# Optimization experiments

Measured on AMD Instinct MI355X. Metric: run time of the kernel, lower is better.

The kernel has to match this reference:

```python
import jax, jax.numpy as jnp
import numpy as np

NA = 100000
NB = 100000
N_REL = 6
REL_SRC = ['A', 'B', 'A', 'B', 'A', 'B']
REL_DST = ['B', 'A', 'A', 'B', 'B', 'A']
N_NODES = {'A': NA, 'B': NB}
H_DIM, OUT_DIM, N_BASES, N_EDGES = 64, 16, 4, 500000


def setup_inputs() -> dict:
    key = jax.random.key(0)
    ks = jax.random.split(key, 16)
    inp = {
        'embed_A': jax.random.normal(ks[0], (NA, H_DIM), jnp.float32) * 0.1,
        'embed_B': jax.random.normal(ks[1], (NB, H_DIM), jnp.float32) * 0.1,
        'bias0': jnp.zeros((H_DIM,), jnp.float32),
        'w_comp1': jax.random.normal(ks[2], (N_REL, N_BASES), jnp.float32) * 0.5,
        'basis1': jax.random.normal(ks[3], (N_BASES, H_DIM, H_DIM), jnp.float32) * (1.0 / np.sqrt(H_DIM)),
        'bias1': jnp.zeros((H_DIM,), jnp.float32),
        'w_comp2': jax.random.normal(ks[4], (N_REL, N_BASES), jnp.float32) * 0.5,
        'basis2': jax.random.normal(ks[5], (N_BASES, H_DIM, OUT_DIM), jnp.float32) * (1.0 / np.sqrt(H_DIM)),
        'bias2': jnp.zeros((OUT_DIM,), jnp.float32),
    }
    for r in range(N_REL):
        inp[f'src_r{r}'] = jax.random.randint(ks[6 + r], (N_EDGES,), 0, N_NODES[REL_SRC[r]], jnp.int32)
        inp[f'dst_r{r}'] = jax.random.randint(jax.random.fold_in(ks[6 + r], 7), (N_EDGES,), 0, N_NODES[REL_DST[r]], jnp.int32)
    return inp


def _hetero_conv(h, W_rels, bias, edges, out_dim, activation):
    # h: dict ntype -> [N, d_in]; W_rels: None or [n_rel, d_in, d_out]
    out = {nt: jnp.zeros((N_NODES[nt], out_dim), h['A'].dtype) for nt in N_NODES}
    for r in range(N_REL):
        src_t, dst_t = REL_SRC[r], REL_DST[r]
        src, dst = edges[r]
        x = h[src_t] if W_rels is None else h[src_t] @ W_rels[r]  # [N_src, d_out]
        msg = x[src]  # gather: [E, d_out]
        n_dst = N_NODES[dst_t]
        agg = jax.ops.segment_sum(msg, dst, num_segments=n_dst)
        deg = jax.ops.segment_sum(jnp.ones((msg.shape[0],), msg.dtype), dst, num_segments=n_dst)
        out[dst_t] = out[dst_t] + agg / jnp.maximum(deg, 1.0)[:, None]  # norm='right'
    out = {nt: out[nt] + bias for nt in out}
    if activation is not None:
        out = {nt: activation(out[nt]) for nt in out}
    return out


def reference(embed_A, embed_B, bias0, w_comp1, basis1, bias1, w_comp2, basis2, bias2,
              src_r0, dst_r0, src_r1, dst_r1, src_r2, dst_r2,
              src_r3, dst_r3, src_r4, dst_r4, src_r5, dst_r5):
    edges = [(src_r0, dst_r0), (src_r1, dst_r1), (src_r2, dst_r2),
             (src_r3, dst_r3), (src_r4, dst_r4), (src_r5, dst_r5)]
    h = {'A': embed_A, 'B': embed_B}
    # layer 0: weight=False -> pure normalized aggregation + bias + relu
    h = _hetero_conv(h, None, bias0, edges, H_DIM, jax.nn.relu)
    # hidden layer with basis-decomposed weights
    W1 = jnp.einsum('rb,bio->rio', w_comp1, basis1)
    h = _hetero_conv(h, W1, bias1, edges, H_DIM, jax.nn.relu)
    # output layer, no activation
    W2 = jnp.einsum('rb,bio->rio', w_comp2, basis2)
    h = _hetero_conv(h, W2, bias2, edges, OUT_DIM, None)
    return h['A']  # logits for category node type
```

## Files before the change

kernel.cpp:

```cpp
#include <hip/hip_runtime.h>

#define NN 100000
#define EE 500000
#define DD 64
#define OD 16
#define NR 6
#define NBASE 4
#define BSH 10
#define NBK 98
#define SBLK 128
#define FLATN (NBK * SBLK)
#define STCAP 5632
#define DBIN 64
#define DBLK 128
#define FLAT2 (DBIN * DBLK)
#define NVR 8

struct Edges { const int* src[NR]; const int* dst[NR]; };

typedef __attribute__((ext_vector_type(8))) short bf16x8;
typedef __attribute__((ext_vector_type(4))) float f32x4;

__device__ __forceinline__ float bf2f(ushort u) {
    union { unsigned int i; float f; } v; v.i = ((unsigned int)u) << 16; return v.f;
}
__device__ __forceinline__ ushort f2bf(float f) {
    unsigned int x = __float_as_uint(f);
    unsigned int r = (x + 0x7fffu + ((x >> 16) & 1u)) >> 16;
    return (ushort)r;
}
__device__ __forceinline__ void bfpair(unsigned int u, float& lo, float& hi) {
    lo = __uint_as_float(u << 16);
    hi = __uint_as_float(u & 0xffff0000u);
}

__global__ __launch_bounds__(256) void build_w_kernel(
    const float* __restrict__ wc1, const float* __restrict__ b1,
    const float* __restrict__ wc2, const float* __restrict__ b2,
    ushort* __restrict__ Wp1, ushort* __restrict__ Wp2)
{
    int idx = blockIdx.x * blockDim.x + threadIdx.x;
    const int n1 = NR * DD * DD;
    const int n2 = NR * DD * OD;
    if (idx < n1) {
        int r = idx >> 12, rem = idx & 4095;
        int i = rem >> 6, o = rem & 63;
        float s = 0.f;
        #pragma unroll
        for (int b = 0; b < NBASE; ++b) s += wc1[r * NBASE + b] * b1[b * 4096 + rem];
        Wp1[(((size_t)(r * 8 + (i >> 3)) * 64 + o) << 3) + (i & 7)] = f2bf(s);
    } else if (idx < n1 + n2) {
        int j = idx - n1;
        int r = j >> 10, rem = j & 1023;
        int i = rem >> 4, o = rem & 15;
        float s = 0.f;
        #pragma unroll
        for (int b = 0; b < NBASE; ++b) s += wc2[r * NBASE + b] * b2[b * 1024 + rem];
        Wp2[(((size_t)(r * 8 + (i >> 3)) * 16 + o) << 3) + (i & 7)] = f2bf(s);
    }
}

__global__ __launch_bounds__(256) void cvt_kernel(
    const float* __restrict__ in, ushort* __restrict__ out, int n4)
{
    int i = blockIdx.x * 256 + threadIdx.x;
    if (i >= n4) return;
    float4 v = ((const float4*)in)[i];
    ushort4 o;
    o.x = f2bf(v.x); o.y = f2bf(v.y); o.z = f2bf(v.z); o.w = f2bf(v.w);
    ((ushort4*)out)[i] = o;
}

__global__ __launch_bounds__(256) void count_kernel(Edges ep, int* __restrict__ cnt_mat)
{
    __shared__ int h[NBK];
    int r = blockIdx.y, blk = blockIdx.x;
    const int* __restrict__ dst = ep.dst[r];
    const int chunk = (EE + SBLK - 1) / SBLK;
    int e0 = blk * chunk, e1 = min(e0 + chunk, EE);
    for (int i = threadIdx.x; i < NBK; i += 256) h[i] = 0;
    __syncthreads();
    for (int e = e0 + threadIdx.x; e < e1; e += 256)
        atomicAdd(&h[dst[e] >> BSH], 1);
    __syncthreads();
    for (int b = threadIdx.x; b < NBK; b += 256)
        cnt_mat[r * FLATN + b * SBLK + blk] = h[b];
}

__global__ __launch_bounds__(1024) void flat_scan_kernel(
    const int* __restrict__ cnt_mat, int* __restrict__ off_flat, int* __restrict__ bbase)
{
    __shared__ int wsum[16];
    const int TPE = 13;
    int r = blockIdx.x;
    int tid = threadIdx.x, lane = tid & 63, wid = tid >> 6;
    int base = tid * TPE;
    int v[TPE];
    int s = 0;
    #pragma unroll
    for (int j = 0; j < TPE; ++j) {
        int i = base + j;
        v[j] = (i < FLATN) ? cnt_mat[r * FLATN + i] : 0;
        s += v[j];
    }
    int si = s;
    #pragma unroll
    for (int off = 1; off < 64; off <<= 1) {
        int t = __shfl_up(si, off);
        if (lane >= off) si += t;
    }
    if (lane == 63) wsum[wid] = si;
    __syncthreads();
    if (wid == 0) {
        int ws = (lane < 16) ? wsum[lane] : 0;
        #pragma unroll
        for (int off = 1; off < 16; off <<= 1) {
            int t = __shfl_up(ws, off);
            if (lane >= off) ws += t;
        }
        if (lane < 16) wsum[lane] = ws;
    }
    __syncthreads();
    int texcl = (wid > 0 ? wsum[wid - 1] : 0) + (si - s);
    int part = 0;
    #pragma unroll
    for (int j = 0; j < TPE; ++j) {
        int i = base + j;
        if (i < FLATN) {
            int o = texcl + part;
            off_flat[r * FLATN + i] = o;
            if ((i & (SBLK - 1)) == 0) bbase[r * (NBK + 1) + (i >> 7)] = o;
        }
        part += v[j];
    }
    if (tid == 0) bbase[r * (NBK + 1) + NBK] = EE;
}

__global__ __launch_bounds__(256) void scatter2_kernel(
    Edges ep, const int* __restrict__ off_flat, unsigned int* __restrict__ ebuf)
{
    __shared__ int goff[NBK];
    __shared__ int lcnt[NBK];
    int r = blockIdx.y, blk = blockIdx.x;
    const int* __restrict__ src = ep.src[r];
    const int* __restrict__ dst = ep.dst[r];
    unsigned int* eb = ebuf + (size_t)r * EE;
    const int chunk = (EE + SBLK - 1) / SBLK;
    int e0 = blk * chunk, e1 = min(e0 + chunk, EE);
    if (threadIdx.x < NBK) {
        goff[threadIdx.x] = off_flat[r * FLATN + threadIdx.x * SBLK + blk];
        lcnt[threadIdx.x] = 0;
    }
    __syncthreads();
    for (int e = e0 + threadIdx.x; e < e1; e += 256) {
        int d = dst[e];
        int b = d >> BSH;
        int pos = goff[b] + atomicAdd(&lcnt[b], 1);
        eb[pos] = (unsigned int)src[e] | ((unsigned int)(d & 1023) << 17);
    }
}

__global__ __launch_bounds__(256) void csr_fine_kernel(
    const unsigned int* __restrict__ ebuf, const int* __restrict__ bbase,
    int* __restrict__ row_ptr, float* __restrict__ inv_deg, int* __restrict__ col_idx)
{
    __shared__ int nh[1024];
    __shared__ int nb[1024];
    __shared__ int wsum4[4];
    __shared__ int stage[STCAP];
    int r = blockIdx.y, b = blockIdx.x;
    int tid = threadIdx.x, lane = tid & 63, wid = tid >> 6;
    int gb = bbase[r * (NBK + 1) + b];
    int ge = bbase[r * (NBK + 1) + b + 1];
    int cnt = ge - gb;
    if (cnt > STCAP) cnt = STCAP;
    const unsigned int* eb = ebuf + (size_t)r * EE + gb;
    #pragma unroll
    for (int j = 0; j < 4; ++j) nh[tid * 4 + j] = 0;
    __syncthreads();
    for (int i = tid; i < cnt; i += 256)
        atomicAdd(&nh[(eb[i] >> 17) & 1023], 1);
    __syncthreads();
    int v0 = nh[tid * 4 + 0], v1 = nh[tid * 4 + 1], v2 = nh[tid * 4 + 2], v3 = nh[tid * 4 + 3];
    int s = v0 + v1 + v2 + v3;
    int si = s;
    #pragma unroll
    for (int off = 1; off < 64; off <<= 1) {
        int t = __shfl_up(si, off);
        if (lane >= off) si += t;
    }
    if (lane == 63) wsum4[wid] = si;
    __syncthreads();
    if (tid == 0) {
        int a = 0;
        #pragma unroll
        for (int k = 0; k < 4; ++k) { int t = wsum4[k]; wsum4[k] = a; a += t; }
    }
    __syncthreads();
    int texcl = wsum4[wid] + (si - s);
    int p0 = texcl, p1 = p0 + v0, p2 = p1 + v1, p3 = p2 + v2;
    nb[tid * 4 + 0] = p0; nb[tid * 4 + 1] = p1; nb[tid * 4 + 2] = p2; nb[tid * 4 + 3] = p3;
    {
        int node0 = b * 1024 + tid * 4;
        int pj[4] = { p0, p1, p2, p3 };
        int vj[4] = { v0, v1, v2, v3 };
        #pragma unroll
        for (int j = 0; j < 4; ++j) {
            int node = node0 + j;
            if (node < NN) {
                row_ptr[r * (NN + 1) + node] = gb + pj[j];
                inv_deg[r * NN + node] = 1.0f / (float)(vj[j] > 1 ? vj[j] : 1);
            }
        }
    }
    if (b == NBK - 1 && tid == 0) row_ptr[r * (NN + 1) + NN] = EE;
    #pragma unroll
    for (int j = 0; j < 4; ++j) nh[tid * 4 + j] = 0;
    __syncthreads();
    for (int i = tid; i < cnt; i += 256) {
        unsigned int w = eb[i];
        int loc = (w >> 17) & 1023;
        int pos = nb[loc] + atomicAdd(&nh[loc], 1);
        stage[pos] = (int)(w & 0x1ffffu);
    }
    __syncthreads();
    int* co = col_idx + (size_t)r * EE + gb;
    for (int i = tid; i < cnt; i += 256) co[i] = stage[i];
}

__device__ __forceinline__ int vdeg(int vr, int n, const int* __restrict__ rp)
{
    if (vr < 6) return rp[vr * (NN + 1) + n + 1] - rp[vr * (NN + 1) + n];
    if (vr == 6)
        return (rp[1 * (NN + 1) + n + 1] - rp[1 * (NN + 1) + n])
             + (rp[2 * (NN + 1) + n + 1] - rp[2 * (NN + 1) + n])
             + (rp[5 * (NN + 1) + n + 1] - rp[5 * (NN + 1) + n]);
    return (rp[0 * (NN + 1) + n + 1] - rp[0 * (NN + 1) + n])
         + (rp[3 * (NN + 1) + n + 1] - rp[3 * (NN + 1) + n])
         + (rp[4 * (NN + 1) + n + 1] - rp[4 * (NN + 1) + n]);
}

__global__ __launch_bounds__(256) void dhist_kernel(
    const int* __restrict__ row_ptr, int* __restrict__ cnt2)
{
    __shared__ int h[DBIN];
    int vr = blockIdx.y, blk = blockIdx.x;
    if (threadIdx.x < DBIN) h[threadIdx.x] = 0;
    __syncthreads();
    const int chunk = (NN + DBLK - 1) / DBLK;
    int n0 = blk * chunk, n1 = min(n0 + chunk, NN);
    for (int n = n0 + threadIdx.x; n < n1; n += 256)
        atomicAdd(&h[min(vdeg(vr, n, row_ptr), DBIN - 1)], 1);
    __syncthreads();
    if (threadIdx.x < DBIN) cnt2[vr * FLAT2 + threadIdx.x * DBLK + blk] = h[threadIdx.x];
}

__global__ __launch_bounds__(1024) void dscan_kernel(
    const int* __restrict__ cnt2, int* __restrict__ off2)
{
    __shared__ int wsum[16];
    const int TPE = 8;
    int vr = blockIdx.x;
    int tid = threadIdx.x, lane = tid & 63, wid = tid >> 6;
    int base = tid * TPE;
    int v[TPE];
    int s = 0;
    #pragma unroll
    for (int j = 0; j < TPE; ++j) { v[j] = cnt2[vr * FLAT2 + base + j]; s += v[j]; }
    int si = s;
    #pragma unroll
    for (int off = 1; off < 64; off <<= 1) {
        int t = __shfl_up(si, off);
        if (lane >= off) si += t;
    }
    if (lane == 63) wsum[wid] = si;
    __syncthreads();
    if (wid == 0) {
        int ws = (lane < 16) ? wsum[lane] : 0;
        #pragma unroll
        for (int off = 1; off < 16; off <<= 1) {
            int t = __shfl_up(ws, off);
            if (lane >= off) ws += t;
        }
        if (lane < 16) wsum[lane] = ws;
    }
    __syncthreads();
    int texcl = (wid > 0 ? wsum[wid - 1] : 0) + (si - s);
    int part = 0;
    #pragma unroll
    for (int j = 0; j < TPE; ++j) {
        off2[vr * FLAT2 + base + j] = texcl + part;
        part += v[j];
    }
}

__global__ __launch_bounds__(256) void dscatter_kernel(
    const int* __restrict__ row_ptr, const int* __restrict__ off2, int* __restrict__ perm)
{
    __shared__ int goff[DBIN];
    __shared__ int lcnt[DBIN];
    int vr = blockIdx.y, blk = blockIdx.x;
    if (threadIdx.x < DBIN) {
        goff[threadIdx.x] = off2[vr * FLAT2 + threadIdx.x * DBLK + blk];
        lcnt[threadIdx.x] = 0;
    }
    __syncthreads();
    const int chunk = (NN + DBLK - 1) / DBLK;
    int n0 = blk * chunk, n1 = min(n0 + chunk, NN);
    for (int n = n0 + threadIdx.x; n < n1; n += 256) {
        int b = min(vdeg(vr, n, row_ptr), DBIN - 1);
        int pos = goff[b] + atomicAdd(&lcnt[b], 1);
        perm[vr * NN + pos] = n;
    }
}

__global__ __launch_bounds__(256) void agg_kernel(
    const ushort* __restrict__ hA, const ushort* __restrict__ hB,
    const int* __restrict__ row_ptr, const int* __restrict__ col_idx,
    const float* __restrict__ inv_deg, const int* __restrict__ perm,
    ushort* __restrict__ zA, ushort* __restrict__ zB)
{
    const int relT[6]   = {1, 2, 5, 0, 3, 4};
    const int srcIsA[6] = {0, 1, 0, 1, 0, 1};
    int y = blockIdx.y;
    int r = relT[y];
    const ushort* F = srcIsA[y] ? hA : hB;
    ushort* z = (y < 3) ? zA : zB;
    int ks = (y < 3) ? y : y - 3;
    int tid = threadIdx.x;
    int wid = tid >> 6, lane = tid & 63;
    int grp = lane >> 3, sub = lane & 7;
    int idx = blockIdx.x * 32 + wid * 8 + grp;
    bool valid = (idx < NN);
    int n = valid ? perm[r * NN + idx] : 0;
    const int* rp = row_ptr + r * (NN + 1);
    const int* ci = col_idx + (size_t)r * EE;
    int s = valid ? rp[n] : 0;
    int e = valid ? rp[n + 1] : 0;
    float a0 = 0.f, a1 = 0.f, a2 = 0.f, a3 = 0.f, a4 = 0.f, a5 = 0.f, a6 = 0.f, a7 = 0.f;
    int t = s;
    for (; t + 2 <= e; t += 2) {
        int c0 = ci[t], c1 = ci[t + 1];
        int4 u = *(const int4*)(F + (size_t)c0 * DD + sub * 8);
        int4 w = *(const int4*)(F + (size_t)c1 * DD + sub * 8);
        float l, h;
        bfpair((unsigned int)u.x, l, h); a0 += l; a1 += h;
        bfpair((unsigned int)u.y, l, h); a2 += l; a3 += h;
        bfpair((unsigned int)u.z, l, h); a4 += l; a5 += h;
        bfpair((unsigned int)u.w, l, h); a6 += l; a7 += h;
        bfpair((unsigned int)w.x, l, h); a0 += l; a1 += h;
        bfpair((unsigned int)w.y, l, h); a2 += l; a3 += h;
        bfpair((unsigned int)w.z, l, h); a4 += l; a5 += h;
        bfpair((unsigned int)w.w, l, h); a6 += l; a7 += h;
    }
    if (t < e) {
        int c0 = ci[t];
        int4 u = *(const int4*)(F + (size_t)c0 * DD + sub * 8);
        float l, h;
        bfpair((unsigned int)u.x, l, h); a0 += l; a1 += h;
        bfpair((unsigned int)u.y, l, h); a2 += l; a3 += h;
        bfpair((unsigned int)u.z, l, h); a4 += l; a5 += h;
        bfpair((unsigned int)u.w, l, h); a6 += l; a7 += h;
    }
    if (valid) {
        float inv = inv_deg[r * NN + n];
        int4 o;
        o.x = (int)((unsigned int)f2bf(a0 * inv) | ((unsigned int)f2bf(a1 * inv) << 16));
        o.y = (int)((unsigned int)f2bf(a2 * inv) | ((unsigned int)f2bf(a3 * inv) << 16));
        o.z = (int)((unsigned int)f2bf(a4 * inv) | ((unsigned int)f2bf(a5 * inv) << 16));
        o.w = (int)((unsigned int)f2bf(a6 * inv) | ((unsigned int)f2bf(a7 * inv) << 16));
        *(int4*)(z + (size_t)n * 192 + ks * 64 + sub * 8) = o;
    }
}

__global__ __launch_bounds__(256) void layer0_kernel(
    const ushort* __restrict__ eA, const ushort* __restrict__ eB,
    const int* __restrict__ row_ptr, const int* __restrict__ col_idx,
    const float* __restrict__ inv_deg, const int* __restrict__ perm,
    const float* __restrict__ bias, ushort* __restrict__ hA, ushort* __restrict__ hB)
{
    int side = blockIdx.y;
    const int relT[2][3] = { {1, 2, 5}, {0, 3, 4} };
    int tid = threadIdx.x;
    int wid = tid >> 6, lane = tid & 63;
    int grp = lane >> 3, sub = lane & 7;
    int idx = blockIdx.x * 32 + wid * 8 + grp;
    bool valid = (idx < NN);
    int n = valid ? perm[(6 + side) * NN + idx] : 0;
    float acc[8];
    {
        float4 b0 = *(const float4*)(bias + sub * 8);
        float4 b1 = *(const float4*)(bias + sub * 8 + 4);
        acc[0] = b0.x; acc[1] = b0.y; acc[2] = b0.z; acc[3] = b0.w;
        acc[4] = b1.x; acc[5] = b1.y; acc[6] = b1.z; acc[7] = b1.w;
    }
    #pragma unroll
    for (int ks = 0; ks < 3; ++ks) {
        int r = relT[side][ks];
        const ushort* F = ((side == 0) == (ks == 1)) ? eA : eB;
        const int* rp = row_ptr + r * (NN + 1);
        const int* ci = col_idx + (size_t)r * EE;
        int s = valid ? rp[n] : 0;
        int e = valid ? rp[n + 1] : 0;
        float a0 = 0.f, a1 = 0.f, a2 = 0.f, a3 = 0.f, a4 = 0.f, a5 = 0.f, a6 = 0.f, a7 = 0.f;
        int t = s;
        for (; t + 2 <= e; t += 2) {
            int c0 = ci[t], c1 = ci[t + 1];
            int4 u = *(const int4*)(F + (size_t)c0 * DD + sub * 8);
            int4 w = *(const int4*)(F + (size_t)c1 * DD + sub * 8);
            float l, h;
            bfpair((unsigned int)u.x, l, h); a0 += l; a1 += h;
            bfpair((unsigned int)u.y, l, h); a2 += l; a3 += h;
            bfpair((unsigned int)u.z, l, h); a4 += l; a5 += h;
            bfpair((unsigned int)u.w, l, h); a6 += l; a7 += h;
            bfpair((unsigned int)w.x, l, h); a0 += l; a1 += h;
            bfpair((unsigned int)w.y, l, h); a2 += l; a3 += h;
            bfpair((unsigned int)w.z, l, h); a4 += l; a5 += h;
            bfpair((unsigned int)w.w, l, h); a6 += l; a7 += h;
        }
        if (t < e) {
            int c0 = ci[t];
            int4 u = *(const int4*)(F + (size_t)c0 * DD + sub * 8);
            float l, h;
            bfpair((unsigned int)u.x, l, h); a0 += l; a1 += h;
            bfpair((unsigned int)u.y, l, h); a2 += l; a3 += h;
            bfpair((unsigned int)u.z, l, h); a4 += l; a5 += h;
            bfpair((unsigned int)u.w, l, h); a6 += l; a7 += h;
        }
        float inv = valid ? inv_deg[r * NN + n] : 0.f;
        acc[0] += a0 * inv; acc[1] += a1 * inv; acc[2] += a2 * inv; acc[3] += a3 * inv;
        acc[4] += a4 * inv; acc[5] += a5 * inv; acc[6] += a6 * inv; acc[7] += a7 * inv;
    }
    if (valid) {
        ushort* h = side ? hB : hA;
        int4 o;
        o.x = (int)((unsigned int)f2bf(fmaxf(acc[0], 0.f)) | ((unsigned int)f2bf(fmaxf(acc[1], 0.f)) << 16));
        o.y = (int)((unsigned int)f2bf(fmaxf(acc[2], 0.f)) | ((unsigned int)f2bf(fmaxf(acc[3], 0.f)) << 16));
        o.z = (int)((unsigned int)f2bf(fmaxf(acc[4], 0.f)) | ((unsigned int)f2bf(fmaxf(acc[5], 0.f)) << 16));
        o.w = (int)((unsigned int)f2bf(fmaxf(acc[6], 0.f)) | ((unsigned int)f2bf(fmaxf(acc[7], 0.f)) << 16));
        *(int4*)(h + (size_t)n * DD + sub * 8) = o;
    }
}

__global__ __launch_bounds__(256) void gemm1_mfma_kernel(
    const ushort* __restrict__ A, const ushort* __restrict__ Wp,
    int r0, int r1, int r2, const float* __restrict__ bias, ushort* __restrict__ out)
{
    int tid = threadIdx.x;
    int wave = tid >> 6, lane = tid & 63;
    int q = lane & 15, p = lane >> 4;
    int n0 = blockIdx.x * 64 + wave * 16;
    int rr[3] = { r0, r1, r2 };
    f32x4 acc0 = {0.f, 0.f, 0.f, 0.f};
    f32x4 acc1 = {0.f, 0.f, 0.f, 0.f};
    f32x4 acc2 = {0.f, 0.f, 0.f, 0.f};
    f32x4 acc3 = {0.f, 0.f, 0.f, 0.f};
    const ushort* arow = A + (size_t)(n0 + q) * 192 + p * 8;
    #pragma unroll
    for (int ks = 0; ks < 3; ++ks) {
        int rel = rr[ks];
        #pragma unroll
        for (int t = 0; t < 2; ++t) {
            bf16x8 a = *(const bf16x8*)(arow + ks * 64 + t * 32);
            const ushort* wb = Wp + (((size_t)(rel * 8 + t * 4 + p) * 64 + q) << 3);
            bf16x8 b0 = *(const bf16x8*)(wb);
            bf16x8 b1 = *(const bf16x8*)(wb + 16 * 8);
            bf16x8 b2 = *(const bf16x8*)(wb + 32 * 8);
            bf16x8 b3 = *(const bf16x8*)(wb + 48 * 8);
            acc0 = __builtin_amdgcn_mfma_f32_16x16x32_bf16(a, b0, acc0, 0, 0, 0);
            acc1 = __builtin_amdgcn_mfma_f32_16x16x32_bf16(a, b1, acc1, 0, 0, 0);
            acc2 = __builtin_amdgcn_mfma_f32_16x16x32_bf16(a, b2, acc2, 0, 0, 0);
            acc3 = __builtin_amdgcn_mfma_f32_16x16x32_bf16(a, b3, acc3, 0, 0, 0);
        }
    }
    float bv0 = bias[q], bv1 = bias[16 + q], bv2 = bias[32 + q], bv3 = bias[48 + q];
    #pragma unroll
    for (int v = 0; v < 4; ++v) {
        int n = n0 + p * 4 + v;
        if (n < NN) {
            ushort* orow = out + (size_t)n * 64;
            orow[q]      = f2bf(fmaxf(acc0[v] + bv0, 0.f));
            orow[16 + q] = f2bf(fmaxf(acc1[v] + bv1, 0.f));
            orow[32 + q] = f2bf(fmaxf(acc2[v] + bv2, 0.f));
            orow[48 + q] = f2bf(fmaxf(acc3[v] + bv3, 0.f));
        }
    }
}

__global__ __launch_bounds__(256) void gemm2_mfma_kernel(
    const ushort* __restrict__ A, const ushort* __restrict__ Wp,
    int r0, int r1, int r2, const float* __restrict__ bias, float* __restrict__ out)
{
    int tid = threadIdx.x;
    int wave = tid >> 6, lane = tid & 63;
    int q = lane & 15, p = lane >> 4;
    int n0 = blockIdx.x * 64 + wave * 16;
    int rr[3] = { r0, r1, r2 };
    f32x4 acc = {0.f, 0.f, 0.f, 0.f};
    const ushort* arow = A + (size_t)(n0 + q) * 192 + p * 8;
    #pragma unroll
    for (int ks = 0; ks < 3; ++ks) {
        int rel = rr[ks];
        #pragma unroll
        for (int t = 0; t < 2; ++t) {
            bf16x8 a = *(const bf16x8*)(arow + ks * 64 + t * 32);
            bf16x8 b = *(const bf16x8*)(Wp + (((size_t)(rel * 8 + t * 4 + p) * 16 + q) << 3));
            acc = __builtin_amdgcn_mfma_f32_16x16x32_bf16(a, b, acc, 0, 0, 0);
        }
    }
    float bv = bias[q];
    #pragma unroll
    for (int v = 0; v < 4; ++v) {
        int n = n0 + p * 4 + v;
        if (n < NN) out[(size_t)n * 16 + q] = acc[v] + bv;
    }
}

extern "C" void kernel_launch(void* const* d_in, const int* in_sizes, int n_in,
                              void* d_out, int out_size, void* d_ws, size_t ws_size,
                              hipStream_t stream)
{
    const float* embA  = (const float*)d_in[0];
    const float* embB  = (const float*)d_in[1];
    const float* bias0 = (const float*)d_in[2];
    const float* wc1   = (const float*)d_in[3];
    const float* b1    = (const float*)d_in[4];
    const float* bias1 = (const float*)d_in[5];
    const float* wc2   = (const float*)d_in[6];
    const float* b2    = (const float*)d_in[7];
    const float* bias2 = (const float*)d_in[8];

    Edges ep;
    for (int r = 0; r < NR; ++r) {
        ep.src[r] = (const int*)d_in[9 + 2 * r];
        ep.dst[r] = (const int*)d_in[10 + 2 * r];
    }

    char* ws = (char*)d_ws;
    size_t off = 0;
    auto alloc = [&](size_t bytes) {
        void* p = ws + off;
        off = (off + bytes + 255) & ~(size_t)255;
        return p;
    };
    ushort* Wp1     = (ushort*)alloc((size_t)NR * 8 * 64 * 8 * 2);
    ushort* Wp2     = (ushort*)alloc((size_t)NR * 8 * 16 * 8 * 2);
    int*    cnt_mat = (int*)   alloc((size_t)NR * FLATN * 4);
    int*    off_fl  = (int*)   alloc((size_t)NR * FLATN * 4);
    int*    bbase   = (int*)   alloc((size_t)NR * (NBK + 1) * 4);
    int*    row_ptr = (int*)   alloc((size_t)NR * (NN + 1) * 4);
    float*  inv_deg = (float*) alloc((size_t)NR * NN * 4);
    int*    col_idx = (int*)   alloc((size_t)NR * EE * 4);
    int*    perm    = (int*)   alloc((size_t)NVR * NN * 4);
    ushort* zA      = (ushort*)alloc((size_t)NN * 192 * 2);
    ushort* zB      = (ushort*)alloc((size_t)NN * 192 * 2);
    ushort* h0A     = (ushort*)alloc((size_t)NN * DD * 2);
    ushort* h0B     = (ushort*)alloc((size_t)NN * DD * 2);
    ushort* h1A     = (ushort*)alloc((size_t)NN * DD * 2);
    ushort* h1B     = (ushort*)alloc((size_t)NN * DD * 2);
    (void)ws_size;

    unsigned int* ebuf   = (unsigned int*)zA;
    ushort*       embA16 = h1A;
    ushort*       embB16 = h1B;
    int*          cnt2   = cnt_mat;
    int*          off2   = off_fl;

    int nw = NR * DD * DD + NR * DD * OD;
    build_w_kernel<<<(nw + 255) / 256, 256, 0, stream>>>(wc1, b1, wc2, b2, Wp1, Wp2);
    cvt_kernel<<<(NN * DD / 4 + 255) / 256, 256, 0, stream>>>(embA, embA16, NN * DD / 4);
    cvt_kernel<<<(NN * DD / 4 + 255) / 256, 256, 0, stream>>>(embB, embB16, NN * DD / 4);

    count_kernel<<<dim3(SBLK, NR), 256, 0, stream>>>(ep, cnt_mat);
    flat_scan_kernel<<<NR, 1024, 0, stream>>>(cnt_mat, off_fl, bbase);
    scatter2_kernel<<<dim3(SBLK, NR), 256, 0, stream>>>(ep, off_fl, ebuf);
    csr_fine_kernel<<<dim3(NBK, NR), 256, 0, stream>>>(ebuf, bbase, row_ptr, inv_deg, col_idx);

    dhist_kernel<<<dim3(DBLK, NVR), 256, 0, stream>>>(row_ptr, cnt2);
    dscan_kernel<<<NVR, 1024, 0, stream>>>(cnt2, off2);
    dscatter_kernel<<<dim3(DBLK, NVR), 256, 0, stream>>>(row_ptr, off2, perm);

    int agx = (NN + 31) / 32;
    int ggrid = (NN + 63) / 64;

    layer0_kernel<<<dim3(agx, 2), 256, 0, stream>>>(
        embA16, embB16, row_ptr, col_idx, inv_deg, perm, bias0, h0A, h0B);

    agg_kernel<<<dim3(agx, 6), 256, 0, stream>>>(
        h0A, h0B, row_ptr, col_idx, inv_deg, perm, zA, zB);
    gemm1_mfma_kernel<<<ggrid, 256, 0, stream>>>(zA, Wp1, 1, 2, 5, bias1, h1A);
    gemm1_mfma_kernel<<<ggrid, 256, 0, stream>>>(zB, Wp1, 0, 3, 4, bias1, h1B);

    agg_kernel<<<dim3(agx, 3), 256, 0, stream>>>(
        h1A, h1B, row_ptr, col_idx, inv_deg, perm, zA, zB);
    gemm2_mfma_kernel<<<ggrid, 256, 0, stream>>>(zA, Wp2, 1, 2, 5, bias2, (float*)d_out);
}
```

Before: 310.7 us.

## Merge launches, replace global degree sort with per-block local sort, unroll gathers by four

```diff
diff --git a/kernel.cpp b/kernel.cpp
--- a/kernel.cpp
+++ b/kernel.cpp
@@ -12,8 +12,6 @@
 #define FLATN (NBK * SBLK)
 #define STCAP 5632
 #define DBIN 64
-#define DBLK 128
-#define FLAT2 (DBIN * DBLK)
 #define NVR 8
 
 struct Edges { const int* src[NR]; const int* dst[NR]; };
@@ -32,6 +30,13 @@
 __device__ __forceinline__ void bfpair(unsigned int u, float& lo, float& hi) {
     lo = __uint_as_float(u << 16);
     hi = __uint_as_float(u & 0xffff0000u);
+}
+__device__ __forceinline__ void acc8(const int4& u, float* a) {
+    float l, h;
+    bfpair((unsigned int)u.x, l, h); a[0] += l; a[1] += h;
+    bfpair((unsigned int)u.y, l, h); a[2] += l; a[3] += h;
+    bfpair((unsigned int)u.z, l, h); a[4] += l; a[5] += h;
+    bfpair((unsigned int)u.w, l, h); a[6] += l; a[7] += h;
 }
 
 __global__ __launch_bounds__(256) void build_w_kernel(
@@ -61,10 +66,13 @@
 }
 
 __global__ __launch_bounds__(256) void cvt_kernel(
-    const float* __restrict__ in, ushort* __restrict__ out, int n4)
+    const float* __restrict__ inA, const float* __restrict__ inB,
+    ushort* __restrict__ outA, ushort* __restrict__ outB, int n4)
 {
     int i = blockIdx.x * 256 + threadIdx.x;
     if (i >= n4) return;
+    const float* in = blockIdx.y ? inB : inA;
+    ushort* out = blockIdx.y ? outB : outA;
     float4 v = ((const float4*)in)[i];
     ushort4 o;
     o.x = f2bf(v.x); o.y = f2bf(v.y); o.z = f2bf(v.z); o.w = f2bf(v.w);
@@ -240,77 +248,45 @@
          + (rp[4 * (NN + 1) + n + 1] - rp[4 * (NN + 1) + n]);
 }
 
-__global__ __launch_bounds__(256) void dhist_kernel(
-    const int* __restrict__ row_ptr, int* __restrict__ cnt2)
+__global__ __launch_bounds__(256) void bsort_kernel(
+    const int* __restrict__ row_ptr, int* __restrict__ perm)
 {
     __shared__ int h[DBIN];
-    int vr = blockIdx.y, blk = blockIdx.x;
-    if (threadIdx.x < DBIN) h[threadIdx.x] = 0;
-    __syncthreads();
-    const int chunk = (NN + DBLK - 1) / DBLK;
-    int n0 = blk * chunk, n1 = min(n0 + chunk, NN);
-    for (int n = n0 + threadIdx.x; n < n1; n += 256)
-        atomicAdd(&h[min(vdeg(vr, n, row_ptr), DBIN - 1)], 1);
-    __syncthreads();
-    if (threadIdx.x < DBIN) cnt2[vr * FLAT2 + threadIdx.x * DBLK + blk] = h[threadIdx.x];
-}
-
-__global__ __launch_bounds__(1024) void dscan_kernel(
-    const int* __restrict__ cnt2, int* __restrict__ off2)
-{
-    __shared__ int wsum[16];
-    const int TPE = 8;
-    int vr = blockIdx.x;
-    int tid = threadIdx.x, lane = tid & 63, wid = tid >> 6;
-    int base = tid * TPE;
-    int v[TPE];
-    int s = 0;
-    #pragma unroll
-    for (int j = 0; j < TPE; ++j) { v[j] = cnt2[vr * FLAT2 + base + j]; s += v[j]; }
-    int si = s;
-    #pragma unroll
-    for (int off = 1; off < 64; off <<= 1) {
-        int t = __shfl_up(si, off);
-        if (lane >= off) si += t;
-    }
-    if (lane == 63) wsum[wid] = si;
-    __syncthreads();
-    if (wid == 0) {
-        int ws = (lane < 16) ? wsum[lane] : 0;
-        #pragma unroll
-        for (int off = 1; off < 16; off <<= 1) {
-            int t = __shfl_up(ws, off);
-            if (lane >= off) ws += t;
-        }
-        if (lane < 16) wsum[lane] = ws;
-    }
-    __syncthreads();
-    int texcl = (wid > 0 ? wsum[wid - 1] : 0) + (si - s);
-    int part = 0;
-    #pragma unroll
-    for (int j = 0; j < TPE; ++j) {
-        off2[vr * FLAT2 + base + j] = texcl + part;
-        part += v[j];
-    }
-}
-
-__global__ __launch_bounds__(256) void dscatter_kernel(
-    const int* __restrict__ row_ptr, const int* __restrict__ off2, int* __restrict__ perm)
-{
-    __shared__ int goff[DBIN];
-    __shared__ int lcnt[DBIN];
-    int vr = blockIdx.y, blk = blockIdx.x;
-    if (threadIdx.x < DBIN) {
-        goff[threadIdx.x] = off2[vr * FLAT2 + threadIdx.x * DBLK + blk];
-        lcnt[threadIdx.x] = 0;
-    }
-    __syncthreads();
-    const int chunk = (NN + DBLK - 1) / DBLK;
-    int n0 = blk * chunk, n1 = min(n0 + chunk, NN);
-    for (int n = n0 + threadIdx.x; n < n1; n += 256) {
-        int b = min(vdeg(vr, n, row_ptr), DBIN - 1);
-        int pos = goff[b] + atomicAdd(&lcnt[b], 1);
-        perm[vr * NN + pos] = n;
+    __shared__ int base_[DBIN];
+    int vr = blockIdx.y, b = blockIdx.x;
+    int n0 = b * 1024;
+    int cnt = min(1024, NN - n0);
+    int tid = threadIdx.x;
+    if (tid < DBIN) h[tid] = 0;
+    __syncthreads();
+    int bin[4];
+    #pragma unroll
+    for (int j = 0; j < 4; ++j) {
+        int i = tid + j * 256;
+        if (i < cnt) {
+            bin[j] = min(vdeg(vr, n0 + i, row_ptr), DBIN - 1);
+            atomicAdd(&h[bin[j]], 1);
+        } else bin[j] = -1;
+    }
+    __syncthreads();
+    if (tid < 64) {
+        int v = h[tid];
+        int s = v;
+        #pragma unroll
+        for (int off = 1; off < 64; off <<= 1) {
+            int t = __shfl_up(s, off);
+            if (tid >= off) s += t;
+        }
+        base_[tid] = s - v;
+        h[tid] = 0;
+    }
+    __syncthreads();
+    #pragma unroll
+    for (int j = 0; j < 4; ++j) {
+        if (bin[j] >= 0) {
+            int pos = base_[bin[j]] + atomicAdd(&h[bin[j]], 1);
+            perm[vr * NN + n0 + pos] = n0 + tid + j * 256;
+        }
     }
 }
 
@@ -337,38 +313,27 @@
     const int* ci = col_idx + (size_t)r * EE;
     int s = valid ? rp[n] : 0;
     int e = valid ? rp[n + 1] : 0;
-    float a0 = 0.f, a1 = 0.f, a2 = 0.f, a3 = 0.f, a4 = 0.f, a5 = 0.f, a6 = 0.f, a7 = 0.f;
+    float a[8] = {0.f, 0.f, 0.f, 0.f, 0.f, 0.f, 0.f, 0.f};
     int t = s;
-    for (; t + 2 <= e; t += 2) {
-        int c0 = ci[t], c1 = ci[t + 1];
-        int4 u = *(const int4*)(F + (size_t)c0 * DD + sub * 8);
-        int4 w = *(const int4*)(F + (size_t)c1 * DD + sub * 8);
-        float l, h;
-        bfpair((unsigned int)u.x, l, h); a0 += l; a1 += h;
-        bfpair((unsigned int)u.y, l, h); a2 += l; a3 += h;
-        bfpair((unsigned int)u.z, l, h); a4 += l; a5 += h;
-        bfpair((unsigned int)u.w, l, h); a6 += l; a7 += h;
-        bfpair((unsigned int)w.x, l, h); a0 += l; a1 += h;
-        bfpair((unsigned int)w.y, l, h); a2 += l; a3 += h;
-        bfpair((unsigned int)w.z, l, h); a4 += l; a5 += h;
-        bfpair((unsigned int)w.w, l, h); a6 += l; a7 += h;
-    }
-    if (t < e) {
-        int c0 = ci[t];
-        int4 u = *(const int4*)(F + (size_t)c0 * DD + sub * 8);
-        float l, h;
-        bfpair((unsigned int)u.x, l, h); a0 += l; a1 += h;
-        bfpair((unsigned int)u.y, l, h); a2 += l; a3 += h;
-        bfpair((unsigned int)u.z, l, h); a4 += l; a5 += h;
-        bfpair((unsigned int)u.w, l, h); a6 += l; a7 += h;
+    for (; t + 4 <= e; t += 4) {
+        int c0 = ci[t], c1 = ci[t + 1], c2 = ci[t + 2], c3 = ci[t + 3];
+        int4 u0 = *(const int4*)(F + (size_t)c0 * DD + sub * 8);
+        int4 u1 = *(const int4*)(F + (size_t)c1 * DD + sub * 8);
+        int4 u2 = *(const int4*)(F + (size_t)c2 * DD + sub * 8);
+        int4 u3 = *(const int4*)(F + (size_t)c3 * DD + sub * 8);
+        acc8(u0, a); acc8(u1, a); acc8(u2, a); acc8(u3, a);
+    }
+    for (; t < e; ++t) {
+        int4 u = *(const int4*)(F + (size_t)ci[t] * DD + sub * 8);
+        acc8(u, a);
     }
     if (valid) {
         float inv = inv_deg[r * NN + n];
         int4 o;
-        o.x = (int)((unsigned int)f2bf(a0 * inv) | ((unsigned int)f2bf(a1 * inv) << 16));
-        o.y = (int)((unsigned int)f2bf(a2 * inv) | ((unsigned int)f2bf(a3 * inv) << 16));
-        o.z = (int)((unsigned int)f2bf(a4 * inv) | ((unsigned int)f2bf(a5 * inv) << 16));
-        o.w = (int)((unsigned int)f2bf(a6 * inv) | ((unsigned int)f2bf(a7 * inv) << 16));
+        o.x = (int)((unsigned int)f2bf(a[0] * inv) | ((unsigned int)f2bf(a[1] * inv) << 16));
+        o.y = (int)((unsigned int)f2bf(a[2] * inv) | ((unsigned int)f2bf(a[3] * inv) << 16));
+        o.z = (int)((unsigned int)f2bf(a[4] * inv) | ((unsigned int)f2bf(a[5] * inv) << 16));
+        o.w = (int)((unsigned int)f2bf(a[6] * inv) | ((unsigned int)f2bf(a[7] * inv) << 16));
         *(int4*)(z + (size_t)n * 192 + ks * 64 + sub * 8) = o;
     }
 }
@@ -402,34 +367,23 @@
         const int* ci = col_idx + (size_t)r * EE;
         int s = valid ? rp[n] : 0;
         int e = valid ? rp[n + 1] : 0;
-        float a0 = 0.f, a1 = 0.f, a2 = 0.f, a3 = 0.f, a4 = 0.f, a5 = 0.f, a6 = 0.f, a7 = 0.f;
+        float a[8] = {0.f, 0.f, 0.f, 0.f, 0.f, 0.f, 0.f, 0.f};
         int t = s;
-        for (; t + 2 <= e; t += 2) {
-            int c0 = ci[t], c1 = ci[t + 1];
-            int4 u = *(const int4*)(F + (size_t)c0 * DD + sub * 8);
-            int4 w = *(const int4*)(F + (size_t)c1 * DD + sub * 8);
-            float l, h;
-            bfpair((unsigned int)u.x, l, h); a0 += l; a1 += h;
-            bfpair((unsigned int)u.y, l, h); a2 += l; a3 += h;
-            bfpair((unsigned int)u.z, l, h); a4 += l; a5 += h;
-            bfpair((unsigned int)u.w, l, h); a6 += l; a7 += h;
-            bfpair((unsigned int)w.x, l, h); a0 += l; a1 += h;
-            bfpair((unsigned int)w.y, l, h); a2 += l; a3 += h;
-            bfpair((unsigned int)w.z, l, h); a4 += l; a5 += h;
-            bfpair((unsigned int)w.w, l, h); a6 += l; a7 += h;
-        }
-        if (t < e) {
-            int c0 = ci[t];
-            int4 u = *(const int4*)(F + (size_t)c0 * DD + sub * 8);
-            float l, h;
-            bfpair((unsigned int)u.x, l, h); a0 += l; a1 += h;
-            bfpair((unsigned int)u.y, l, h); a2 += l; a3 += h;
-            bfpair((unsigned int)u.z, l, h); a4 += l; a5 += h;
-            bfpair((unsigned int)u.w, l, h); a6 += l; a7 += h;
+        for (; t + 4 <= e; t += 4) {
+            int c0 = ci[t], c1 = ci[t + 1], c2 = ci[t + 2], c3 = ci[t + 3];
+            int4 u0 = *(const int4*)(F + (size_t)c0 * DD + sub * 8);
+            int4 u1 = *(const int4*)(F + (size_t)c1 * DD + sub * 8);
+            int4 u2 = *(const int4*)(F + (size_t)c2 * DD + sub * 8);
+            int4 u3 = *(const int4*)(F + (size_t)c3 * DD + sub * 8);
+            acc8(u0, a); acc8(u1, a); acc8(u2, a); acc8(u3, a);
+        }
+        for (; t < e; ++t) {
+            int4 u = *(const int4*)(F + (size_t)ci[t] * DD + sub * 8);
+            acc8(u, a);
         }
         float inv = valid ? inv_deg[r * NN + n] : 0.f;
-        acc[0] += a0 * inv; acc[1] += a1 * inv; acc[2] += a2 * inv; acc[3] += a3 * inv;
-        acc[4] += a4 * inv; acc[5] += a5 * inv; acc[6] += a6 * inv; acc[7] += a7 * inv;
+        #pragma unroll
+        for (int j = 0; j < 8; ++j) acc[j] += a[j] * inv;
     }
     if (valid) {
         ushort* h = side ? hB : hA;
@@ -443,14 +397,18 @@
 }
 
 __global__ __launch_bounds__(256) void gemm1_mfma_kernel(
-    const ushort* __restrict__ A, const ushort* __restrict__ Wp,
-    int r0, int r1, int r2, const float* __restrict__ bias, ushort* __restrict__ out)
-{
+    const ushort* __restrict__ zA, const ushort* __restrict__ zB,
+    const ushort* __restrict__ Wp, const float* __restrict__ bias,
+    ushort* __restrict__ hA, ushort* __restrict__ hB)
+{
+    const int relT[2][3] = { {1, 2, 5}, {0, 3, 4} };
+    int y = blockIdx.y;
+    const ushort* A = y ? zB : zA;
+    ushort* out = y ? hB : hA;
     int tid = threadIdx.x;
     int wave = tid >> 6, lane = tid & 63;
     int q = lane & 15, p = lane >> 4;
     int n0 = blockIdx.x * 64 + wave * 16;
-    int rr[3] = { r0, r1, r2 };
     f32x4 acc0 = {0.f, 0.f, 0.f, 0.f};
     f32x4 acc1 = {0.f, 0.f, 0.f, 0.f};
     f32x4 acc2 = {0.f, 0.f, 0.f, 0.f};
@@ -458,7 +416,7 @@
     const ushort* arow = A + (size_t)(n0 + q) * 192 + p * 8;
     #pragma unroll
     for (int ks = 0; ks < 3; ++ks) {
-        int rel = rr[ks];
+        int rel = relT[y][ks];
         #pragma unroll
         for (int t = 0; t < 2; ++t) {
             bf16x8 a = *(const bf16x8*)(arow + ks * 64 + t * 32);
@@ -563,22 +521,18 @@
     unsigned int* ebuf   = (unsigned int*)zA;
     ushort*       embA16 = h1A;
     ushort*       embB16 = h1B;
-    int*          cnt2   = cnt_mat;
-    int*          off2   = off_fl;
 
     int nw = NR * DD * DD + NR * DD * OD;
     build_w_kernel<<<(nw + 255) / 256, 256, 0, stream>>>(wc1, b1, wc2, b2, Wp1, Wp2);
-    cvt_kernel<<<(NN * DD / 4 + 255) / 256, 256, 0, stream>>>(embA, embA16, NN * DD / 4);
-    cvt_kernel<<<(NN * DD / 4 + 255) / 256, 256, 0, stream>>>(embB, embB16, NN * DD / 4);
+    cvt_kernel<<<dim3((NN * DD / 4 + 255) / 256, 2), 256, 0, stream>>>(
+        embA, embB, embA16, embB16, NN * DD / 4);
 
     count_kernel<<<dim3(SBLK, NR), 256, 0, stream>>>(ep, cnt_mat);
     flat_scan_kernel<<<NR, 1024, 0, stream>>>(cnt_mat, off_fl, bbase);
     scatter2_kernel<<<dim3(SBLK, NR), 256, 0, stream>>>(ep, off_fl, ebuf);
     csr_fine_kernel<<<dim3(NBK, NR), 256, 0, stream>>>(ebuf, bbase, row_ptr, inv_deg, col_idx);
 
-    dhist_kernel<<<dim3(DBLK, NVR), 256, 0, stream>>>(row_ptr, cnt2);
-    dscan_kernel<<<NVR, 1024, 0, stream>>>(cnt2, off2);
-    dscatter_kernel<<<dim3(DBLK, NVR), 256, 0, stream>>>(row_ptr, off2, perm);
+    bsort_kernel<<<dim3(NBK, NVR), 256, 0, stream>>>(row_ptr, perm);
 
     int agx = (NN + 31) / 32;
     int ggrid = (NN + 63) / 64;
@@ -588,8 +542,8 @@
 
     agg_kernel<<<dim3(agx, 6), 256, 0, stream>>>(
         h0A, h0B, row_ptr, col_idx, inv_deg, perm, zA, zB);
-    gemm1_mfma_kernel<<<ggrid, 256, 0, stream>>>(zA, Wp1, 1, 2, 5, bias1, h1A);
-    gemm1_mfma_kernel<<<ggrid, 256, 0, stream>>>(zB, Wp1, 0, 3, 4, bias1, h1B);
+    gemm1_mfma_kernel<<<dim3(ggrid, 2), 256, 0, stream>>>(
+        zA, zB, Wp1, bias1, h1A, h1B);
 
     agg_kernel<<<dim3(agx, 3), 256, 0, stream>>>(
         h1A, h1B, row_ptr, col_idx, inv_deg, perm, zA, zB);
```

Result: faster. 303.1 us (-2.4%).
